# Optimization experiments

Measured on AMD Instinct MI355X. Metric: run time of the kernel, lower is better.

## Reference

```python
import jax, jax.numpy as jnp
import numpy as np

N, E, IN_DIM, H, OUT, MAPD = 20000, 640000, 24, 128, 24, 512
SLOPE = 0.01  # torch F.leaky_relu default


def setup_inputs() -> dict:
    key = jax.random.key(0)
    ks = jax.random.split(key, 20)
    g = lambda i, shape, s: jax.random.normal(ks[i], shape, jnp.float32) * s
    inp = {
        "feats": g(0, (N, IN_DIM), 1.0),
        "e_w": jax.random.uniform(ks[1], (E, 1), dtype=jnp.float32),
        "maps_embedding": g(2, (N, MAPD), 1.0),
        "snorm_n": jnp.ones((N, 1), jnp.float32),
        "src": jax.random.randint(ks[3], (E,), 0, N),
        "dst": jax.random.randint(ks[4], (E,), 0, N),
        "W_eh": g(5, (H, IN_DIM), (2.0 / IN_DIM) ** 0.5), "b_eh": jnp.zeros((H,), jnp.float32),
        "W_ee": g(6, (H, 1), 1.0), "b_ee": jnp.zeros((H,), jnp.float32),
        "W_cat": g(7, (H, H + MAPD), (2.0 / (H + MAPD)) ** 0.5), "b_cat": jnp.zeros((H,), jnp.float32),
        "Ws1": g(8, (H, H), (2.0 / H) ** 0.5), "Wf1": g(9, (H, H), (2.0 / H) ** 0.5),
        "a1": g(10, (2 * H,), (2.0 / (2 * H)) ** 0.5),
        "Ws2": g(11, (H, H), (2.0 / H) ** 0.5), "Wf2": g(12, (H, H), (2.0 / H) ** 0.5),
        "a2": g(13, (2 * H,), (2.0 / (2 * H)) ** 0.5),
        "W_out": g(14, (OUT, H), (2.0 / H) ** 0.5), "b_out": jnp.zeros((OUT,), jnp.float32),
    }
    return inp


def gat_layer(h, src, dst, Ws, Wf, a):
    # My_GATLayer with (as constructed in My_GAT) relu=False, att_ew=False, dropouts=0.
    h_in = h
    h_s = h @ Ws.T                         # [N,H] self transform
    z = h @ Wf.T                           # [N,H] message transform
    # attention score = leaky_relu(a^T [z_src, z_dst]) computed via per-node halves
    s_src = z @ a[:H]                      # [N]
    s_dst = z @ a[H:]                      # [N]
    e = jax.nn.leaky_relu(s_src[src] + s_dst[dst], SLOPE)          # [E]
    # numerically stable segment softmax over incoming edges grouped by dst
    m = jax.ops.segment_max(e, dst, num_segments=N)
    m = jnp.where(jnp.isfinite(m), m, 0.0)
    ex = jnp.exp(e - m[dst])
    denom = jax.ops.segment_sum(ex, dst, num_segments=N)
    alpha = ex / jnp.maximum(denom[dst], 1e-16)                    # [E]
    agg = jax.ops.segment_sum(alpha[:, None] * z[src], dst, num_segments=N)  # [N,H]
    indeg = jax.ops.segment_sum(jnp.ones_like(e), dst, num_segments=N)
    # DGL update_all leaves zero-in-degree nodes at their prior ndata['h'] (= h_in)
    h_node = jnp.where(indeg[:, None] > 0, h_s + agg, h_in)
    return h_in + h_node                   # residual connection; relu disabled (positional-arg bug)


def reference(feats, e_w, maps_embedding, snorm_n, src, dst,
              W_eh, b_eh, W_ee, b_ee, W_cat, b_cat,
              Ws1, Wf1, a1, Ws2, Wf2, a2, W_out, b_out):
    feats = feats.reshape(feats.shape[0], -1)
    h = feats @ W_eh.T + b_eh                                  # embedding_h
    _e = e_w @ W_ee.T + b_ee                                   # edge embedding (stored on g.edata['w'], unused since att_ew binds to attn_drop)
    h = jnp.concatenate([maps_embedding, h], axis=-1) @ W_cat.T + b_cat
    h = jax.nn.relu(h)
    h = gat_layer(h, src, dst, Ws1, Wf1, a1)
    h = gat_layer(h, src, dst, Ws2, Wf2, a2)
    return h @ W_out.T + b_out
```

## Files before the change

kernel.cpp:

```cpp
#include <hip/hip_runtime.h>

#define HBLK 128
#define EPB 4096

typedef __attribute__((ext_vector_type(8))) short s8v;
typedef __attribute__((ext_vector_type(4))) float f32x4;
typedef __attribute__((ext_vector_type(8))) _Float16 h8f;

__device__ inline void split2(float x, short& h, short& l) {
    unsigned hb = __float_as_uint(x) & 0xFFFF0000u;
    float hf = __uint_as_float(hb);
    float lf = x - hf;
    h = (short)(hb >> 16);
    l = (short)(__float_as_uint(lf) >> 16);
}

__device__ inline void split8(const float4& a0, const float4& a1, s8v& ah, s8v& al) {
    float vv[8];
    *(float4*)&vv[0] = a0;
    *(float4*)&vv[4] = a1;
#pragma unroll
    for (int e = 0; e < 8; ++e) {
        short hh, ll;
        split2(vv[e], hh, ll);
        ah[e] = hh;
        al[e] = ll;
    }
}


__global__ void bin_hist(const int* __restrict__ dst, int* __restrict__ histT,
                         int E, int NB1) {
    __shared__ int h[256];
    const int t = threadIdx.x, blk = blockIdx.x;
    h[t] = 0;
    __syncthreads();
    const int e0 = blk * EPB;
    const int e1 = min(E, e0 + EPB);
    for (int e = e0 + t; e < e1; e += 256)
        atomicAdd(&h[dst[e] >> 7], 1);
    __syncthreads();
    histT[t * NB1 + blk] = h[t];
}

__global__ void scan1(const int* __restrict__ counts, int* __restrict__ offs,
                      int* __restrict__ bsums, int n) {
    __shared__ int lds[256];
    const int t = threadIdx.x;
    const int i = blockIdx.x * 256 + t;
    const int v = (i < n) ? counts[i] : 0;
    lds[t] = v;
    __syncthreads();
    for (int off = 1; off < 256; off <<= 1) {
        int add = (t >= off) ? lds[t - off] : 0;
        __syncthreads();
        lds[t] += add;
        __syncthreads();
    }
    if (i < n) offs[i] = lds[t] - v;
    if (t == 255) bsums[blockIdx.x] = lds[255];
}

__global__ void scan2(int* __restrict__ bsums, int nb) {
    __shared__ int lds[256];
    const int t = threadIdx.x;
    const int v = (t < nb) ? bsums[t] : 0;
    lds[t] = v;
    __syncthreads();
    for (int off = 1; off < 256; off <<= 1) {
        int add = (t >= off) ? lds[t - off] : 0;
        __syncthreads();
        lds[t] += add;
        __syncthreads();
    }
    if (t < nb) bsums[t] = lds[t] - v;
}

__global__ void bin_scatter(const int* __restrict__ src, const int* __restrict__ dst,
                            const int* __restrict__ histT, const int* __restrict__ bsums,
                            int* __restrict__ ebuf, int E, int NB1) {
    __shared__ int cur[256];
    const int t = threadIdx.x, blk = blockIdx.x;
    const int li = t * NB1 + blk;
    cur[t] = histT[li] + bsums[li >> 8];
    __syncthreads();
    const int e0 = blk * EPB;
    const int e1 = min(E, e0 + EPB);
    for (int e = e0 + t; e < e1; e += 256) {
        const int d = dst[e];
        const int p = atomicAdd(&cur[d >> 7], 1);
        ebuf[p] = (src[e] << 7) | (d & 127);
    }
}

__global__ void bucket_sort(const int* __restrict__ ebuf, const int* __restrict__ histT,
                            const int* __restrict__ bsums,
                            int* __restrict__ offs, int* __restrict__ srcs,
                            int N, int E, int NB1) {
    __shared__ int cnt[256];
    __shared__ int cur[256];
    const int t = threadIdx.x, b = blockIdx.x;
    const int li0 = b * NB1;
    const int ebase = histT[li0] + bsums[li0 >> 8];
    int eend = E;
    if (b + 1 < 256) {
        const int li1 = (b + 1) * NB1;
        eend = histT[li1] + bsums[li1 >> 8];
    }
    cnt[t] = 0;
    __syncthreads();
    for (int e = ebase + t; e < eend; e += 256)
        atomicAdd(&cnt[ebuf[e] & 127], 1);
    __syncthreads();
    const int own = cnt[t];
    for (int off = 1; off < 256; off <<= 1) {
        int add = (t >= off) ? cnt[t - off] : 0;
        __syncthreads();
        cnt[t] += add;
        __syncthreads();
    }
    const int excl = cnt[t] - own;
    cur[t] = ebase + excl;
    const int node = (b << 7) + t;
    if (t < 128 && node < N) offs[node] = ebase + excl;
    if (b == 0 && t == 0) offs[N] = E;
    __syncthreads();
    for (int e = ebase + t; e < eend; e += 256) {
        const int ed = ebuf[e];
        const int p = atomicAdd(&cur[ed & 127], 1);
        srcs[p] = ed >> 7;
    }
}

__global__ void pack_wcat(const float* __restrict__ Wcat, int ldw, int mapd,
                          const float* __restrict__ Weh, int indim,
                          const float* __restrict__ beh, const float* __restrict__ bcat,
                          short* __restrict__ dh, short* __restrict__ dl,
                          float* __restrict__ bcomb, int K) {
    const long i = (long)blockIdx.x * 256 + threadIdx.x;
    const long total = (long)HBLK * K;
    if (i < total) {
        const int c = (int)(i / K), k = (int)(i % K);
        float x = 0.f;
        if (k < mapd) {
            x = Wcat[(long)c * ldw + k];
        } else if (k < mapd + indim) {
            const float* wc = Wcat + (long)c * ldw + mapd;
            const int kk = k - mapd;
            float s = 0.f;
            for (int j = 0; j < HBLK; ++j) s += wc[j] * Weh[j * indim + kk];
            x = s;
        }
        short h, l;
        split2(x, h, l);
        const int j = c >> 4, l16 = c & 15;
        const int chunk = k >> 5, quad = (k >> 3) & 3, t = k & 7;
        const long off = (((long)(chunk * 8 + j) * 64) + quad * 16 + l16) * 8 + t;
        dh[off] = h;
        dl[off] = l;
    } else if (i < total + HBLK) {
        const int c = (int)(i - total);
        const float* wc = Wcat + (long)c * ldw + mapd;
        float s = bcat[c];
        for (int j = 0; j < HBLK; ++j) s += wc[j] * beh[j];
        bcomb[c] = s;
    }
}

__global__ void split_w_packA(const float* __restrict__ W0, const float* __restrict__ W1,
                              const float* __restrict__ W2, const float* __restrict__ W3,
                              const float* __restrict__ Wout, int outd,
                              short* __restrict__ dh, short* __restrict__ dl,
                              short* __restrict__ doh, short* __restrict__ dol) {
    const int m = blockIdx.y;
    const long i = (long)blockIdx.x * 256 + threadIdx.x;
    if (m < 4) {
        const float* Ws[4] = {W0, W1, W2, W3};
        const int c = (int)(i >> 7), k = (int)(i & 127);
        float x = Ws[m][c * HBLK + k];
        short h, l;
        split2(x, h, l);
        const int j = c >> 4, l16 = c & 15;
        const int chunk = k >> 5, quad = (k >> 3) & 3, t = k & 7;
        const long off = (long)m * 16384 + (((long)(chunk * 8 + j) * 64) + quad * 16 + l16) * 8 + t;
        dh[off] = h;
        dl[off] = l;
    } else {
        if (i >= 32 * HBLK) return;
        const int c = (int)(i >> 7), k = (int)(i & 127);
        float x = (c < outd) ? Wout[c * HBLK + k] : 0.f;
        short h, l;
        split2(x, h, l);
        const int j = c >> 4, l16 = c & 15;
        const int chunk = k >> 5, quad = (k >> 3) & 3, t = k & 7;
        const long off = (((long)(chunk * 2 + j) * 64) + quad * 16 + l16) * 8 + t;
        doh[off] = h;
        dol[off] = l;
    }
}

__global__ __launch_bounds__(256, 2) void gemm_bigk(
    const float* __restrict__ A1, int lda1, int K1,
    const float* __restrict__ A2, int lda2, int Kin,
    int K,
    const short* __restrict__ Wh, const short* __restrict__ Wl,
    const float* __restrict__ bias,
    float* __restrict__ Cf, int M)
{
    __shared__ short lds_h[2][4096];
    __shared__ short lds_l[2][4096];
    const int tid = threadIdx.x;
    const int wv = tid >> 6;
    const int lane = tid & 63;
    const int l16 = lane & 15;
    const int quad = lane >> 4;
    const int m0 = blockIdx.x * 64 + wv * 16;
    int ra = m0 + l16;
    if (ra >= M) ra = M - 1;
    const long r1 = (long)ra * lda1;
    const long r2 = (long)ra * lda2;
    const int NC = K >> 5;

    f32x4 acc[8];
#pragma unroll
    for (int j = 0; j < 8; ++j) acc[j] = (f32x4){0.f, 0.f, 0.f, 0.f};

#define LOAD_A(d0, d1, kb)                                      \
    {                                                           \
        const int col0 = (kb) + quad * 8;                       \
        if (col0 < K1) {                                        \
            const float* ap = A1 + r1 + col0;                   \
            d0 = *(const float4*)ap;                            \
            d1 = *(const float4*)(ap + 4);                      \
        } else if (col0 < Kin) {                                \
            const float* ap = A2 + r2 + (col0 - K1);            \
            d0 = *(const float4*)ap;                            \
            d1 = *(const float4*)(ap + 4);                      \
        } else {                                                \
            d0 = make_float4(0.f, 0.f, 0.f, 0.f);               \
            d1 = make_float4(0.f, 0.f, 0.f, 0.f);               \
        }                                                       \
    }
#define LOAD_W(r0, r1w, r2w, r3, c)                             \
    {                                                           \
        const int4* gh = (const int4*)(Wh + (long)(c) * 4096);  \
        const int4* gl = (const int4*)(Wl + (long)(c) * 4096);  \
        r0 = gh[tid * 2]; r1w = gh[tid * 2 + 1];                \
        r2w = gl[tid * 2]; r3 = gl[tid * 2 + 1];                \
    }
#define WRITE_W(b, r0, r1w, r2w, r3)                            \
    {                                                           \
        int4* bh = (int4*)lds_h[b];                             \
        int4* bl = (int4*)lds_l[b];                             \
        bh[tid * 2] = r0; bh[tid * 2 + 1] = r1w;                \
        bl[tid * 2] = r2w; bl[tid * 2 + 1] = r3;                \
    }

    int4 wa0, wa1, wa2, wa3, wb0, wb1, wb2, wb3;
    LOAD_W(wa0, wa1, wa2, wa3, 0)
    WRITE_W(0, wa0, wa1, wa2, wa3)
    LOAD_W(wa0, wa1, wa2, wa3, 1)
    LOAD_W(wb0, wb1, wb2, wb3, 2)
    float4 a0c, a1c, a0n, a1n, a0p, a1p;
    float4 a0q = make_float4(0.f, 0.f, 0.f, 0.f);
    float4 a1q = make_float4(0.f, 0.f, 0.f, 0.f);
    LOAD_A(a0c, a1c, 0)
    LOAD_A(a0n, a1n, 32)
    LOAD_A(a0p, a1p, 64)
    asm volatile("s_waitcnt lgkmcnt(0)" ::: "memory");
    __builtin_amdgcn_s_barrier();
    asm volatile("" ::: "memory");

    for (int c = 0; c < NC; ++c) {
        const int nb = c & 1;
        if (c + 3 < NC) {
            LOAD_A(a0q, a1q, (c + 3) * 32)
        }
        s8v ah, al;
        split8(a0c, a1c, ah, al);
#pragma unroll
        for (int j = 0; j < 8; ++j) {
            const s8v whf = *(const s8v*)&lds_h[nb][(j * 64 + lane) * 8];
            const s8v wlf = *(const s8v*)&lds_l[nb][(j * 64 + lane) * 8];
            acc[j] = __builtin_amdgcn_mfma_f32_16x16x32_bf16(ah, whf, acc[j], 0, 0, 0);
            acc[j] = __builtin_amdgcn_mfma_f32_16x16x32_bf16(ah, wlf, acc[j], 0, 0, 0);
            acc[j] = __builtin_amdgcn_mfma_f32_16x16x32_bf16(al, whf, acc[j], 0, 0, 0);
        }
        if (c + 1 < NC) {
            WRITE_W(nb ^ 1, wa0, wa1, wa2, wa3)
            wa0 = wb0; wa1 = wb1; wa2 = wb2; wa3 = wb3;
            if (c + 3 < NC) LOAD_W(wb0, wb1, wb2, wb3, c + 3)
            asm volatile("s_waitcnt lgkmcnt(0)" ::: "memory");
            __builtin_amdgcn_s_barrier();
            asm volatile("" ::: "memory");
        }
        a0c = a0n; a1c = a1n;
        a0n = a0p; a1n = a1p;
        a0p = a0q; a1p = a1q;
    }
#undef LOAD_A
#undef LOAD_W
#undef WRITE_W

#pragma unroll
    for (int r = 0; r < 4; ++r) {
        const int gr = m0 + quad * 4 + r;
        if (gr >= M) continue;
#pragma unroll
        for (int j = 0; j < 8; ++j) {
            const int col = j * 16 + l16;
            float v = acc[j][r] + bias[col];
            Cf[(long)gr * HBLK + col] = fmaxf(v, 0.f);
        }
    }
}

__global__ __launch_bounds__(256, 2) void gemm_smallk(
    const float* __restrict__ A,
    const short* __restrict__ W1h, const short* __restrict__ W1l,
    const short* __restrict__ W2h, const short* __restrict__ W2l,
    float* __restrict__ C1f, _Float16* __restrict__ Czh,
    const float* __restrict__ avec,
    float* __restrict__ sOut, float* __restrict__ dOut, int M)
{
    __shared__ short lh[16384];
    __shared__ short ll[16384];
    const short* __restrict__ Wh = blockIdx.y ? W2h : W1h;
    const short* __restrict__ Wl = blockIdx.y ? W2l : W1l;
    float* __restrict__ Cf = blockIdx.y ? nullptr : C1f;
    _Float16* __restrict__ Ch16 = blockIdx.y ? Czh : nullptr;
    const float* __restrict__ av = blockIdx.y ? avec : nullptr;
    const int tid = threadIdx.x;
    const int wv = tid >> 6;
    const int lane = tid & 63;
    const int l16 = lane & 15;
    const int quad = lane >> 4;
    const int m0 = blockIdx.x * 64 + wv * 16;
    int ra = m0 + l16;
    if (ra >= M) ra = M - 1;
    const float* arow = A + (long)ra * HBLK + quad * 8;

    {
        const int4* gh = (const int4*)Wh;
        const int4* gl = (const int4*)Wl;
        int4* bh = (int4*)lh;
        int4* bl = (int4*)ll;
#pragma unroll
        for (int i = 0; i < 8; ++i) {
            bh[i * 256 + tid] = gh[i * 256 + tid];
            bl[i * 256 + tid] = gl[i * 256 + tid];
        }
    }
    float4 aw0[4], aw1[4];
#pragma unroll
    for (int c = 0; c < 4; ++c) {
        aw0[c] = *(const float4*)(arow + c * 32);
        aw1[c] = *(const float4*)(arow + c * 32 + 4);
    }
    f32x4 acc[8];
#pragma unroll
    for (int j = 0; j < 8; ++j) acc[j] = (f32x4){0.f, 0.f, 0.f, 0.f};
    __syncthreads();

#pragma unroll
    for (int c = 0; c < 4; ++c) {
        s8v ah, al;
        split8(aw0[c], aw1[c], ah, al);
#pragma unroll
        for (int j = 0; j < 8; ++j) {
            const s8v whf = *(const s8v*)&lh[((c * 8 + j) * 64 + lane) * 8];
            const s8v wlf = *(const s8v*)&ll[((c * 8 + j) * 64 + lane) * 8];
            acc[j] = __builtin_amdgcn_mfma_f32_16x16x32_bf16(ah, whf, acc[j], 0, 0, 0);
            acc[j] = __builtin_amdgcn_mfma_f32_16x16x32_bf16(ah, wlf, acc[j], 0, 0, 0);
            acc[j] = __builtin_amdgcn_mfma_f32_16x16x32_bf16(al, whf, acc[j], 0, 0, 0);
        }
    }

#pragma unroll
    for (int r = 0; r < 4; ++r) {
        const int gr = m0 + quad * 4 + r;
        if (gr >= M) continue;
#pragma unroll
        for (int j = 0; j < 8; ++j) {
            const int col = j * 16 + l16;
            const float v = acc[j][r];
            if (Cf) Cf[(long)gr * HBLK + col] = v;
            if (Ch16) Ch16[(long)gr * HBLK + col] = (_Float16)v;
        }
    }

    if (av) {
        float av0[8], av1[8];
#pragma unroll
        for (int j = 0; j < 8; ++j) {
            av0[j] = av[j * 16 + l16];
            av1[j] = av[128 + j * 16 + l16];
        }
#pragma unroll
        for (int r = 0; r < 4; ++r) {
            float ssp = 0.f, sdp = 0.f;
#pragma unroll
            for (int j = 0; j < 8; ++j) {
                const float v = acc[j][r];
                ssp += v * av0[j];
                sdp += v * av1[j];
            }
#pragma unroll
            for (int off = 1; off < 16; off <<= 1) {
                ssp += __shfl_xor(ssp, off);
                sdp += __shfl_xor(sdp, off);
            }
            const int gr = m0 + quad * 4 + r;
            if (l16 == 0 && gr < M) {
                sOut[gr] = ssp;
                dOut[gr] = sdp;
            }
        }
    }
}

__global__ __launch_bounds__(256) void gemm_out(
    const float* __restrict__ A,
    const short* __restrict__ Wh, const short* __restrict__ Wl,
    const float* __restrict__ bias, float* __restrict__ out,
    int M, int OUTD)
{
    __shared__ short lh[4096], ll[4096];
    const int tid = threadIdx.x;
    {
        const int4* gh = (const int4*)Wh;
        const int4* gl = (const int4*)Wl;
        int4* bh = (int4*)lh;
        int4* bl = (int4*)ll;
        bh[tid * 2] = gh[tid * 2];
        bh[tid * 2 + 1] = gh[tid * 2 + 1];
        bl[tid * 2] = gl[tid * 2];
        bl[tid * 2 + 1] = gl[tid * 2 + 1];
    }
    const int wv = tid >> 6;
    const int lane = tid & 63;
    const int l16 = lane & 15;
    const int quad = lane >> 4;
    const int m0 = blockIdx.x * 64 + wv * 16;
    int ra = m0 + l16;
    if (ra >= M) ra = M - 1;
    const float* arow = A + (long)ra * HBLK + quad * 8;

    f32x4 acc[2];
    acc[0] = (f32x4){0.f, 0.f, 0.f, 0.f};
    acc[1] = (f32x4){0.f, 0.f, 0.f, 0.f};
    __syncthreads();

#pragma unroll
    for (int c = 0; c < 4; ++c) {
        const float4 a0 = *(const float4*)(arow + c * 32);
        const float4 a1 = *(const float4*)(arow + c * 32 + 4);
        s8v ah, al;
        split8(a0, a1, ah, al);
#pragma unroll
        for (int j = 0; j < 2; ++j) {
            const s8v whf = *(const s8v*)&lh[((c * 2 + j) * 64 + lane) * 8];
            const s8v wlf = *(const s8v*)&ll[((c * 2 + j) * 64 + lane) * 8];
            acc[j] = __builtin_amdgcn_mfma_f32_16x16x32_bf16(ah, whf, acc[j], 0, 0, 0);
            acc[j] = __builtin_amdgcn_mfma_f32_16x16x32_bf16(ah, wlf, acc[j], 0, 0, 0);
            acc[j] = __builtin_amdgcn_mfma_f32_16x16x32_bf16(al, whf, acc[j], 0, 0, 0);
        }
    }

#pragma unroll
    for (int r = 0; r < 4; ++r) {
        const int gr = m0 + quad * 4 + r;
        if (gr >= M) continue;
#pragma unroll
        for (int j = 0; j < 2; ++j) {
            const int col = j * 16 + l16;
            if (col < OUTD)
                out[(long)gr * OUTD + col] = acc[j][r] + bias[col];
        }
    }
}

__global__ void gat_gather(const float* __restrict__ h_in, const float* __restrict__ hs,
                           const _Float16* __restrict__ zh,
                           const float* __restrict__ s_src, const float* __restrict__ s_dst,
                           const int* __restrict__ offs, const int* __restrict__ srcs,
                           float* __restrict__ h_out, int N) {
    const int wave = threadIdx.x >> 6;
    const int lane = threadIdx.x & 63;
    const int n = blockIdx.x * 4 + wave;
    if (n >= N) return;
    const int g = lane >> 4, l = lane & 15;
    const int beg = offs[n], end = offs[n + 1];
    const int deg = end - beg;

    float acc[8] = {};
    if (deg > 0) {
        const float sd = s_dst[n];
        if (deg <= 64) {
            const int sA = srcs[beg + min(lane, deg - 1)];
            float e = sd + s_src[sA];
            e = e > 0.f ? e : 0.01f * e;
            if (lane >= deg) e = -INFINITY;
            float mv = e;
#pragma unroll
            for (int off = 32; off; off >>= 1) mv = fmaxf(mv, __shfl_xor(mv, off));
            const float ex = (lane < deg) ? __expf(e - mv) : 0.f;
            float sv = ex;
#pragma unroll
            for (int off = 32; off; off >>= 1) sv += __shfl_xor(sv, off);
            const float w = ex / fmaxf(sv, 1e-16f);

            const int nK = (deg + 3) >> 2;
            int k = 0;
            for (; k + 1 < nK; k += 2) {
                const int i0 = 4 * k + g;
                const int i1 = i0 + 4;
                const int s0 = __shfl(sA, i0);
                const int s1 = __shfl(sA, i1);
                const float w0 = __shfl(w, i0);
                const float w1 = __shfl(w, i1);
                const h8f z0 = *(const h8f*)(zh + (long)s0 * HBLK + 8 * l);
                const h8f z1 = *(const h8f*)(zh + (long)s1 * HBLK + 8 * l);
#pragma unroll
                for (int e2 = 0; e2 < 8; ++e2)
                    acc[e2] += w0 * (float)z0[e2] + w1 * (float)z1[e2];
            }
            if (k < nK) {
                const int i0 = 4 * k + g;
                const int s0 = __shfl(sA, i0);
                const float w0 = __shfl(w, i0);
                const h8f z0 = *(const h8f*)(zh + (long)s0 * HBLK + 8 * l);
#pragma unroll
                for (int e2 = 0; e2 < 8; ++e2)
                    acc[e2] += w0 * (float)z0[e2];
            }
        } else {
            float m = -INFINITY, s = 0.f;
            for (int i = beg + lane; i < end; i += 64) {
                float e = sd + s_src[srcs[i]];
                e = e > 0.f ? e : 0.01f * e;
                float nm = fmaxf(m, e);
                s = s * __expf(m - nm) + __expf(e - nm);
                m = nm;
            }
#pragma unroll
            for (int off = 32; off > 0; off >>= 1) {
                float m2 = __shfl_down(m, off);
                float s2 = __shfl_down(s, off);
                if (m2 > m) {
                    float t = m; m = m2; m2 = t;
                    float ts = s; s = s2; s2 = ts;
                }
                s = (m == -INFINITY) ? 0.f : s + s2 * __expf(m2 - m);
            }
            m = __shfl(m, 0);
            s = __shfl(s, 0);
            const float inv = 1.f / fmaxf(s, 1e-16f);
            for (int i = beg + g; i < end; i += 4) {
                const int s0 = srcs[i];
                float e0 = sd + s_src[s0];
                e0 = e0 > 0.f ? e0 : 0.01f * e0;
                const float w0 = __expf(e0 - m) * inv;
                const h8f z0 = *(const h8f*)(zh + (long)s0 * HBLK + 8 * l);
#pragma unroll
                for (int e2 = 0; e2 < 8; ++e2)
                    acc[e2] += w0 * (float)z0[e2];
            }
        }
#pragma unroll
        for (int e2 = 0; e2 < 8; ++e2) {
            acc[e2] += __shfl_down(acc[e2], 32);
            acc[e2] += __shfl_down(acc[e2], 16);
        }
    }

    if (g == 0) {
        const long base = (long)n * HBLK + 8 * l;
        const float4 hi0 = *(const float4*)(h_in + base);
        const float4 hi1 = *(const float4*)(h_in + base + 4);
        float o[8];
        if (deg > 0) {
            const float4 hv0 = *(const float4*)(hs + base);
            const float4 hv1 = *(const float4*)(hs + base + 4);
            const float* hip = (const float*)&hi0;
            const float* hvp = (const float*)&hv0;
#pragma unroll
            for (int e = 0; e < 4; ++e) o[e] = hip[e] + hvp[e] + acc[e];
            const float* hip1 = (const float*)&hi1;
            const float* hvp1 = (const float*)&hv1;
#pragma unroll
            for (int e = 0; e < 4; ++e) o[4 + e] = hip1[e] + hvp1[e] + acc[4 + e];
        } else {
            const float* hip = (const float*)&hi0;
            const float* hip1 = (const float*)&hi1;
#pragma unroll
            for (int e = 0; e < 4; ++e) o[e] = 2.f * hip[e];
#pragma unroll
            for (int e = 0; e < 4; ++e) o[4 + e] = 2.f * hip1[e];
        }
        *(float4*)(h_out + base) = *(float4*)&o[0];
        *(float4*)(h_out + base + 4) = *(float4*)&o[4];
    }
}

extern "C" void kernel_launch(void* const* d_in, const int* in_sizes, int n_in,
                              void* d_out, int out_size, void* d_ws, size_t ws_size,
                              hipStream_t stream) {
    const float* feats = (const float*)d_in[0];
    const float* maps  = (const float*)d_in[2];
    const int* src = (const int*)d_in[4];
    const int* dst = (const int*)d_in[5];
    const float* W_eh  = (const float*)d_in[6];
    const float* b_eh  = (const float*)d_in[7];
    const float* W_cat = (const float*)d_in[10];
    const float* b_cat = (const float*)d_in[11];
    const float* Ws1 = (const float*)d_in[12];
    const float* Wf1 = (const float*)d_in[13];
    const float* a1  = (const float*)d_in[14];
    const float* Ws2 = (const float*)d_in[15];
    const float* Wf2 = (const float*)d_in[16];
    const float* a2  = (const float*)d_in[17];
    const float* W_out = (const float*)d_in[18];
    const float* b_out = (const float*)d_in[19];

    const int N = in_sizes[3];
    const int E = in_sizes[4];
    const int IN_DIM = in_sizes[0] / N;
    const int MAPD = in_sizes[2] / N;
    const int OUTD = in_sizes[19];
    const int KCAT = MAPD + HBLK;
    const int KC = (MAPD + IN_DIM + 31) & ~31;

    char* p = (char*)d_ws;
    const size_t NH = (size_t)N * HBLK;
    float* hin  = (float*)p;  p += NH * 4;
    float* hs   = (float*)p;  p += NH * 4;
    float* hout = (float*)p;  p += NH * 4;
    _Float16* zh = (_Float16*)p; p += NH * 2;
    float* ssrc = (float*)p;  p += (size_t)N * 4;
    float* sdst = (float*)p;  p += (size_t)N * 4;
    int* offs   = (int*)p;    p += (size_t)(N + 1) * 4;
    int* srcs   = (int*)p;    p += (size_t)E * 4;
    int* bsums  = (int*)p;    p += 256 * 4;
    int* histT  = (int*)p;    p += (size_t)256 * 256 * 4;
    float* bcomb = (float*)p; p += (size_t)HBLK * 4;
    p = (char*)(((uintptr_t)p + 15) & ~(uintptr_t)15);
    int* ebuf = (int*)p;      p += (size_t)E * 4;
    short* Wcat_h = (short*)p; p += (size_t)HBLK * KC * 2;
    short* Wcat_l = (short*)p; p += (size_t)HBLK * KC * 2;
    short* Wout_h = (short*)p; p += (size_t)32 * HBLK * 2;
    short* Wout_l = (short*)p; p += (size_t)32 * HBLK * 2;
    short* Wly_h = (short*)p;  p += (size_t)4 * HBLK * HBLK * 2;
    short* Wly_l = (short*)p;  p += (size_t)4 * HBLK * HBLK * 2;

    const int NB1 = (E + EPB - 1) / EPB;
    const int NBUCK = (N + 127) >> 7;
    const int nHist = 256 * NB1;
    bin_hist<<<NB1, 256, 0, stream>>>(dst, histT, E, NB1);
    scan1<<<NB1, 256, 0, stream>>>(histT, histT, bsums, nHist);
    scan2<<<1, 256, 0, stream>>>(bsums, NB1);
    bin_scatter<<<NB1, 256, 0, stream>>>(src, dst, histT, bsums, ebuf, E, NB1);
    bucket_sort<<<NBUCK, 256, 0, stream>>>(ebuf, histT, bsums, offs, srcs, N, E, NB1);

    pack_wcat<<<(HBLK * KC + HBLK + 255) / 256, 256, 0, stream>>>(
        W_cat, KCAT, MAPD, W_eh, IN_DIM, b_eh, b_cat, Wcat_h, Wcat_l, bcomb, KC);
    split_w_packA<<<dim3(64, 5), 256, 0, stream>>>(
        Ws1, Wf1, Ws2, Wf2, W_out, OUTD, Wly_h, Wly_l, Wout_h, Wout_l);

    const int gGrid = (N + 63) / 64;
    const int n4 = (N + 3) / 4;

    gemm_bigk<<<gGrid, 256, 0, stream>>>(
        maps, MAPD, MAPD, feats, IN_DIM, MAPD + IN_DIM, KC,
        Wcat_h, Wcat_l, bcomb, hin, N);

    gemm_smallk<<<dim3(gGrid, 2), 256, 0, stream>>>(
        hin, Wly_h, Wly_l, Wly_h + 16384, Wly_l + 16384,
        hs, zh, a1, ssrc, sdst, N);
    gat_gather<<<n4, 256, 0, stream>>>(hin, hs, zh, ssrc, sdst, offs, srcs, hout, N);

    gemm_smallk<<<dim3(gGrid, 2), 256, 0, stream>>>(
        hout, Wly_h + 32768, Wly_l + 32768, Wly_h + 49152, Wly_l + 49152,
        hs, zh, a2, ssrc, sdst, N);
    gat_gather<<<n4, 256, 0, stream>>>(hout, hs, zh, ssrc, sdst, offs, srcs, hin, N);

    gemm_out<<<gGrid, 256, 0, stream>>>(hin, Wout_h, Wout_l, b_out, (float*)d_out, N, OUTD);
}
```

Before: 260.8 us.

## Fuse output projection into final gather and merge layer GEMMs per block

Three fusions. The two weight-packing kernels become one launch. Each layer's two GEMMs (self and message transforms) now run in one block: the A tile is split once and reused, with the second weight matrix staged through registers into LDS. The final output projection moves into the last GAT gather kernel as an FP32 dot product against W_out staged in LDS, which drops one kernel launch and the write and re-read of the final hidden state. The cost is half as many GEMM blocks (less parallelism), more register pressure, and a per-block W_out LDS load in the gather kernel.

New measurement: 261.2 us. About the same (+0.2%).

```diff
diff --git a/kernel.cpp b/kernel.cpp
--- a/kernel.cpp
+++ b/kernel.cpp
@@ -132,49 +132,18 @@
     }
 }
 
-__global__ void pack_wcat(const float* __restrict__ Wcat, int ldw, int mapd,
-                          const float* __restrict__ Weh, int indim,
-                          const float* __restrict__ beh, const float* __restrict__ bcat,
-                          short* __restrict__ dh, short* __restrict__ dl,
-                          float* __restrict__ bcomb, int K) {
-    const long i = (long)blockIdx.x * 256 + threadIdx.x;
-    const long total = (long)HBLK * K;
-    if (i < total) {
-        const int c = (int)(i / K), k = (int)(i % K);
-        float x = 0.f;
-        if (k < mapd) {
-            x = Wcat[(long)c * ldw + k];
-        } else if (k < mapd + indim) {
-            const float* wc = Wcat + (long)c * ldw + mapd;
-            const int kk = k - mapd;
-            float s = 0.f;
-            for (int j = 0; j < HBLK; ++j) s += wc[j] * Weh[j * indim + kk];
-            x = s;
-        }
-        short h, l;
-        split2(x, h, l);
-        const int j = c >> 4, l16 = c & 15;
-        const int chunk = k >> 5, quad = (k >> 3) & 3, t = k & 7;
-        const long off = (((long)(chunk * 8 + j) * 64) + quad * 16 + l16) * 8 + t;
-        dh[off] = h;
-        dl[off] = l;
-    } else if (i < total + HBLK) {
-        const int c = (int)(i - total);
-        const float* wc = Wcat + (long)c * ldw + mapd;
-        float s = bcat[c];
-        for (int j = 0; j < HBLK; ++j) s += wc[j] * beh[j];
-        bcomb[c] = s;
-    }
-}
-
-__global__ void split_w_packA(const float* __restrict__ W0, const float* __restrict__ W1,
-                              const float* __restrict__ W2, const float* __restrict__ W3,
-                              const float* __restrict__ Wout, int outd,
-                              short* __restrict__ dh, short* __restrict__ dl,
-                              short* __restrict__ doh, short* __restrict__ dol) {
+__global__ void pack_all(const float* __restrict__ W0, const float* __restrict__ W1,
+                         const float* __restrict__ W2, const float* __restrict__ W3,
+                         short* __restrict__ dh, short* __restrict__ dl,
+                         const float* __restrict__ Wcat, int ldw, int mapd,
+                         const float* __restrict__ Weh, int indim,
+                         const float* __restrict__ beh, const float* __restrict__ bcat,
+                         short* __restrict__ ch, short* __restrict__ cl,
+                         float* __restrict__ bcomb, int K) {
     const int m = blockIdx.y;
     const long i = (long)blockIdx.x * 256 + threadIdx.x;
     if (m < 4) {
+        if (blockIdx.x >= 64) return;
         const float* Ws[4] = {W0, W1, W2, W3};
         const int c = (int)(i >> 7), k = (int)(i & 127);
         float x = Ws[m][c * HBLK + k];
@@ -186,16 +155,33 @@
         dh[off] = h;
         dl[off] = l;
     } else {
-        if (i >= 32 * HBLK) return;
-        const int c = (int)(i >> 7), k = (int)(i & 127);
-        float x = (c < outd) ? Wout[c * HBLK + k] : 0.f;
-        short h, l;
-        split2(x, h, l);
-        const int j = c >> 4, l16 = c & 15;
-        const int chunk = k >> 5, quad = (k >> 3) & 3, t = k & 7;
-        const long off = (((long)(chunk * 2 + j) * 64) + quad * 16 + l16) * 8 + t;
-        doh[off] = h;
-        dol[off] = l;
+        const long total = (long)HBLK * K;
+        if (i < total) {
+            const int c = (int)(i / K), k = (int)(i % K);
+            float x = 0.f;
+            if (k < mapd) {
+                x = Wcat[(long)c * ldw + k];
+            } else if (k < mapd + indim) {
+                const float* wc = Wcat + (long)c * ldw + mapd;
+                const int kk = k - mapd;
+                float s = 0.f;
+                for (int j = 0; j < HBLK; ++j) s += wc[j] * Weh[j * indim + kk];
+                x = s;
+            }
+            short h, l;
+            split2(x, h, l);
+            const int j = c >> 4, l16 = c & 15;
+            const int chunk = k >> 5, quad = (k >> 3) & 3, t = k & 7;
+            const long off = (((long)(chunk * 8 + j) * 64) + quad * 16 + l16) * 8 + t;
+            ch[off] = h;
+            cl[off] = l;
+        } else if (i < total + HBLK) {
+            const int c = (int)(i - total);
+            const float* wc = Wcat + (long)c * ldw + mapd;
+            float s = bcat[c];
+            for (int j = 0; j < HBLK; ++j) s += wc[j] * beh[j];
+            bcomb[c] = s;
+        }
     }
 }
 
@@ -315,21 +301,16 @@
     }
 }
 
-__global__ __launch_bounds__(256, 2) void gemm_smallk(
+__global__ __launch_bounds__(256, 2) void gemm_layer(
     const float* __restrict__ A,
-    const short* __restrict__ W1h, const short* __restrict__ W1l,
-    const short* __restrict__ W2h, const short* __restrict__ W2l,
-    float* __restrict__ C1f, _Float16* __restrict__ Czh,
+    const short* __restrict__ Wsh, const short* __restrict__ Wsl,
+    const short* __restrict__ Wfh, const short* __restrict__ Wfl,
+    float* __restrict__ hsOut, _Float16* __restrict__ zOut,
     const float* __restrict__ avec,
     float* __restrict__ sOut, float* __restrict__ dOut, int M)
 {
     __shared__ short lh[16384];
     __shared__ short ll[16384];
-    const short* __restrict__ Wh = blockIdx.y ? W2h : W1h;
-    const short* __restrict__ Wl = blockIdx.y ? W2l : W1l;
-    float* __restrict__ Cf = blockIdx.y ? nullptr : C1f;
-    _Float16* __restrict__ Ch16 = blockIdx.y ? Czh : nullptr;
-    const float* __restrict__ av = blockIdx.y ? avec : nullptr;
     const int tid = threadIdx.x;
     const int wv = tid >> 6;
     const int lane = tid & 63;
@@ -341,8 +322,8 @@
     const float* arow = A + (long)ra * HBLK + quad * 8;
 
     {
-        const int4* gh = (const int4*)Wh;
-        const int4* gl = (const int4*)Wl;
+        const int4* gh = (const int4*)Wfh;
+        const int4* gl = (const int4*)Wfl;
         int4* bh = (int4*)lh;
         int4* bl = (int4*)ll;
 #pragma unroll
@@ -357,44 +338,52 @@
         aw0[c] = *(const float4*)(arow + c * 32);
         aw1[c] = *(const float4*)(arow + c * 32 + 4);
     }
+    int4 wsh[8], wsl[8];
+    {
+        const int4* gh = (const int4*)Wsh;
+        const int4* gl = (const int4*)Wsl;
+#pragma unroll
+        for (int i = 0; i < 8; ++i) {
+            wsh[i] = gh[i * 256 + tid];
+            wsl[i] = gl[i * 256 + tid];
+        }
+    }
+    s8v ahf[4], alf[4];
+#pragma unroll
+    for (int c = 0; c < 4; ++c) split8(aw0[c], aw1[c], ahf[c], alf[c]);
+
     f32x4 acc[8];
 #pragma unroll
     for (int j = 0; j < 8; ++j) acc[j] = (f32x4){0.f, 0.f, 0.f, 0.f};
-    __syncthreads();
+    asm volatile("s_waitcnt lgkmcnt(0)" ::: "memory");
+    __builtin_amdgcn_s_barrier();
+    asm volatile("" ::: "memory");
 
 #pragma unroll
     for (int c = 0; c < 4; ++c) {
-        s8v ah, al;
-        split8(aw0[c], aw1[c], ah, al);
 #pragma unroll
         for (int j = 0; j < 8; ++j) {
             const s8v whf = *(const s8v*)&lh[((c * 8 + j) * 64 + lane) * 8];
             const s8v wlf = *(const s8v*)&ll[((c * 8 + j) * 64 + lane) * 8];
-            acc[j] = __builtin_amdgcn_mfma_f32_16x16x32_bf16(ah, whf, acc[j], 0, 0, 0);
-            acc[j] = __builtin_amdgcn_mfma_f32_16x16x32_bf16(ah, wlf, acc[j], 0, 0, 0);
-            acc[j] = __builtin_amdgcn_mfma_f32_16x16x32_bf16(al, whf, acc[j], 0, 0, 0);
-        }
-    }
-
+            acc[j] = __builtin_amdgcn_mfma_f32_16x16x32_bf16(ahf[c], whf, acc[j], 0, 0, 0);
+            acc[j] = __builtin_amdgcn_mfma_f32_16x16x32_bf16(ahf[c], wlf, acc[j], 0, 0, 0);
+            acc[j] = __builtin_amdgcn_mfma_f32_16x16x32_bf16(alf[c], whf, acc[j], 0, 0, 0);
+        }
+    }
 #pragma unroll
     for (int r = 0; r < 4; ++r) {
         const int gr = m0 + quad * 4 + r;
         if (gr >= M) continue;
 #pragma unroll
+        for (int j = 0; j < 8; ++j)
+            zOut[(long)gr * HBLK + j * 16 + l16] = (_Float16)acc[j][r];
+    }
+    {
+        float av0[8], av1[8];
+#pragma unroll
         for (int j = 0; j < 8; ++j) {
-            const int col = j * 16 + l16;
-            const float v = acc[j][r];
-            if (Cf) Cf[(long)gr * HBLK + col] = v;
-            if (Ch16) Ch16[(long)gr * HBLK + col] = (_Float16)v;
-        }
-    }
-
-    if (av) {
-        float av0[8], av1[8];
-#pragma unroll
-        for (int j = 0; j < 8; ++j) {
-            av0[j] = av[j * 16 + l16];
-            av1[j] = av[128 + j * 16 + l16];
+            av0[j] = avec[j * 16 + l16];
+            av1[j] = avec[128 + j * 16 + l16];
         }
 #pragma unroll
         for (int r = 0; r < 4; ++r) {
@@ -417,76 +406,63 @@
             }
         }
     }
-}
-
-__global__ __launch_bounds__(256) void gemm_out(
-    const float* __restrict__ A,
-    const short* __restrict__ Wh, const short* __restrict__ Wl,
-    const float* __restrict__ bias, float* __restrict__ out,
-    int M, int OUTD)
-{
-    __shared__ short lh[4096], ll[4096];
-    const int tid = threadIdx.x;
+
+    asm volatile("s_waitcnt lgkmcnt(0)" ::: "memory");
+    __builtin_amdgcn_s_barrier();
+    asm volatile("" ::: "memory");
     {
-        const int4* gh = (const int4*)Wh;
-        const int4* gl = (const int4*)Wl;
         int4* bh = (int4*)lh;
         int4* bl = (int4*)ll;
-        bh[tid * 2] = gh[tid * 2];
-        bh[tid * 2 + 1] = gh[tid * 2 + 1];
-        bl[tid * 2] = gl[tid * 2];
-        bl[tid * 2 + 1] = gl[tid * 2 + 1];
-    }
-    const int wv = tid >> 6;
-    const int lane = tid & 63;
-    const int l16 = lane & 15;
-    const int quad = lane >> 4;
-    const int m0 = blockIdx.x * 64 + wv * 16;
-    int ra = m0 + l16;
-    if (ra >= M) ra = M - 1;
-    const float* arow = A + (long)ra * HBLK + quad * 8;
-
-    f32x4 acc[2];
-    acc[0] = (f32x4){0.f, 0.f, 0.f, 0.f};
-    acc[1] = (f32x4){0.f, 0.f, 0.f, 0.f};
-    __syncthreads();
-
+#pragma unroll
+        for (int i = 0; i < 8; ++i) {
+            bh[i * 256 + tid] = wsh[i];
+            bl[i * 256 + tid] = wsl[i];
+        }
+    }
+    asm volatile("s_waitcnt lgkmcnt(0)" ::: "memory");
+    __builtin_amdgcn_s_barrier();
+    asm volatile("" ::: "memory");
+
+#pragma unroll
+    for (int j = 0; j < 8; ++j) acc[j] = (f32x4){0.f, 0.f, 0.f, 0.f};
 #pragma unroll
     for (int c = 0; c < 4; ++c) {
-        const float4 a0 = *(const float4*)(arow + c * 32);
-        const float4 a1 = *(const float4*)(arow + c * 32 + 4);
-        s8v ah, al;
-        split8(a0, a1, ah, al);
-#pragma unroll
-        for (int j = 0; j < 2; ++j) {
-            const s8v whf = *(const s8v*)&lh[((c * 2 + j) * 64 + lane) * 8];
-            const s8v wlf = *(const s8v*)&ll[((c * 2 + j) * 64 + lane) * 8];
-            acc[j] = __builtin_amdgcn_mfma_f32_16x16x32_bf16(ah, whf, acc[j], 0, 0, 0);
-            acc[j] = __builtin_amdgcn_mfma_f32_16x16x32_bf16(ah, wlf, acc[j], 0, 0, 0);
-            acc[j] = __builtin_amdgcn_mfma_f32_16x16x32_bf16(al, whf, acc[j], 0, 0, 0);
-        }
-    }
-
+#pragma unroll
+        for (int j = 0; j < 8; ++j) {
+            const s8v whf = *(const s8v*)&lh[((c * 8 + j) * 64 + lane) * 8];
+            const s8v wlf = *(const s8v*)&ll[((c * 8 + j) * 64 + lane) * 8];
+            acc[j] = __builtin_amdgcn_mfma_f32_16x16x32_bf16(ahf[c], whf, acc[j], 0, 0, 0);
+            acc[j] = __builtin_amdgcn_mfma_f32_16x16x32_bf16(ahf[c], wlf, acc[j], 0, 0, 0);
+            acc[j] = __builtin_amdgcn_mfma_f32_16x16x32_bf16(alf[c], whf, acc[j], 0, 0, 0);
+        }
+    }
 #pragma unroll
     for (int r = 0; r < 4; ++r) {
         const int gr = m0 + quad * 4 + r;
         if (gr >= M) continue;
 #pragma unroll
-        for (int j = 0; j < 2; ++j) {
-            const int col = j * 16 + l16;
-            if (col < OUTD)
-                out[(long)gr * OUTD + col] = acc[j][r] + bias[col];
-        }
-    }
-}
-
+        for (int j = 0; j < 8; ++j)
+            hsOut[(long)gr * HBLK + j * 16 + l16] = acc[j][r];
+    }
+}
+
+template <int FOUT>
 __global__ void gat_gather(const float* __restrict__ h_in, const float* __restrict__ hs,
                            const _Float16* __restrict__ zh,
                            const float* __restrict__ s_src, const float* __restrict__ s_dst,
                            const int* __restrict__ offs, const int* __restrict__ srcs,
-                           float* __restrict__ h_out, int N) {
-    const int wave = threadIdx.x >> 6;
-    const int lane = threadIdx.x & 63;
+                           float* __restrict__ h_out,
+                           const float* __restrict__ Wout, const float* __restrict__ bout,
+                           float* __restrict__ outp, int OUTD, int N) {
+    __shared__ float wlds[FOUT ? (32 * 132 + 4 * 132) : 4];
+    const int tid = threadIdx.x;
+    const int wave = tid >> 6;
+    const int lane = tid & 63;
+    if constexpr (FOUT) {
+        for (int i = tid; i < OUTD * HBLK; i += 256)
+            wlds[(i >> 7) * 132 + (i & 127)] = Wout[i];
+        __syncthreads();
+    }
     const int n = blockIdx.x * 4 + wave;
     if (n >= N) return;
     const int g = lane >> 4, l = lane & 15;
@@ -598,8 +574,28 @@
 #pragma unroll
             for (int e = 0; e < 4; ++e) o[4 + e] = 2.f * hip1[e];
         }
-        *(float4*)(h_out + base) = *(float4*)&o[0];
-        *(float4*)(h_out + base + 4) = *(float4*)&o[4];
+        if constexpr (FOUT) {
+            float* hr = wlds + 32 * 132 + wave * 132;
+            *(float4*)&hr[8 * l] = *(float4*)&o[0];
+            *(float4*)&hr[8 * l + 4] = *(float4*)&o[4];
+        } else {
+            *(float4*)(h_out + base) = *(float4*)&o[0];
+            *(float4*)(h_out + base + 4) = *(float4*)&o[4];
+        }
+    }
+    if constexpr (FOUT) {
+        if (lane < OUTD) {
+            const float* hr = wlds + 32 * 132 + wave * 132;
+            const float* wr = wlds + lane * 132;
+            float a = bout[lane];
+#pragma unroll 8
+            for (int k = 0; k < 32; ++k) {
+                const float4 hv = *(const float4*)&hr[k * 4];
+                const float4 wv = *(const float4*)&wr[k * 4];
+                a += hv.x * wv.x + hv.y * wv.y + hv.z * wv.z + hv.w * wv.w;
+            }
+            outp[(long)n * OUTD + lane] = a;
+        }
     }
 }
 
@@ -648,8 +644,6 @@
     int* ebuf = (int*)p;      p += (size_t)E * 4;
     short* Wcat_h = (short*)p; p += (size_t)HBLK * KC * 2;
     short* Wcat_l = (short*)p; p += (size_t)HBLK * KC * 2;
-    short* Wout_h = (short*)p; p += (size_t)32 * HBLK * 2;
-    short* Wout_l = (short*)p; p += (size_t)32 * HBLK * 2;
     short* Wly_h = (short*)p;  p += (size_t)4 * HBLK * HBLK * 2;
     short* Wly_l = (short*)p;  p += (size_t)4 * HBLK * HBLK * 2;
 
@@ -662,10 +656,10 @@
     bin_scatter<<<NB1, 256, 0, stream>>>(src, dst, histT, bsums, ebuf, E, NB1);
     bucket_sort<<<NBUCK, 256, 0, stream>>>(ebuf, histT, bsums, offs, srcs, N, E, NB1);
 
-    pack_wcat<<<(HBLK * KC + HBLK + 255) / 256, 256, 0, stream>>>(
+    const int nbW = (HBLK * KC + HBLK + 255) / 256;
+    pack_all<<<dim3(nbW, 5), 256, 0, stream>>>(
+        Ws1, Wf1, Ws2, Wf2, Wly_h, Wly_l,
         W_cat, KCAT, MAPD, W_eh, IN_DIM, b_eh, b_cat, Wcat_h, Wcat_l, bcomb, KC);
-    split_w_packA<<<dim3(64, 5), 256, 0, stream>>>(
-        Ws1, Wf1, Ws2, Wf2, W_out, OUTD, Wly_h, Wly_l, Wout_h, Wout_l);
 
     const int gGrid = (N + 63) / 64;
     const int n4 = (N + 3) / 4;
@@ -674,15 +668,15 @@
         maps, MAPD, MAPD, feats, IN_DIM, MAPD + IN_DIM, KC,
         Wcat_h, Wcat_l, bcomb, hin, N);
 
-    gemm_smallk<<<dim3(gGrid, 2), 256, 0, stream>>>(
+    gemm_layer<<<gGrid, 256, 0, stream>>>(
         hin, Wly_h, Wly_l, Wly_h + 16384, Wly_l + 16384,
         hs, zh, a1, ssrc, sdst, N);
-    gat_gather<<<n4, 256, 0, stream>>>(hin, hs, zh, ssrc, sdst, offs, srcs, hout, N);
-
-    gemm_smallk<<<dim3(gGrid, 2), 256, 0, stream>>>(
+    gat_gather<0><<<n4, 256, 0, stream>>>(hin, hs, zh, ssrc, sdst, offs, srcs, hout,
+                                          nullptr, nullptr, nullptr, OUTD, N);
+
+    gemm_layer<<<gGrid, 256, 0, stream>>>(
         hout, Wly_h + 32768, Wly_l + 32768, Wly_h + 49152, Wly_l + 49152,
         hs, zh, a2, ssrc, sdst, N);
-    gat_gather<<<n4, 256, 0, stream>>>(hout, hs, zh, ssrc, sdst, offs, srcs, hin, N);
-
-    gemm_out<<<gGrid, 256, 0, stream>>>(hin, Wout_h, Wout_l, b_out, (float*)d_out, N, OUTD);
-}
+    gat_gather<1><<<n4, 256, 0, stream>>>(hout, hs, zh, ssrc, sdst, offs, srcs, nullptr,
+                                          W_out, b_out, (float*)d_out, OUTD, N);
+}
```
